# Kernel optimization log

Measured on AMD Instinct MI355X. Metric: run time of the kernel, lower is better.

Reference implementation:

```python
import jax, jax.numpy as jnp
import numpy as np
import math

B, S, D, H = 4, 2048, 1024, 16
DH = D // H  # 64


def setup_inputs() -> dict:
    key = jax.random.key(0)
    ks = jax.random.split(key, 7)
    scale = 1.0 / math.sqrt(D)
    q = jax.random.normal(ks[0], (B, S, D), dtype=jnp.float32)
    k = jax.random.normal(ks[1], (B, S, D), dtype=jnp.float32)
    v = jax.random.normal(ks[2], (B, S, D), dtype=jnp.float32)
    mask = jnp.tril(jnp.ones((S, S), dtype=jnp.int32))[None, None]  # [1,1,S,S] causal
    wq = jax.random.normal(ks[3], (D, D), dtype=jnp.float32) * scale
    wk = jax.random.normal(ks[4], (D, D), dtype=jnp.float32) * scale
    wv = jax.random.normal(ks[5], (D, D), dtype=jnp.float32) * scale
    wo = jax.random.normal(ks[6], (D, D), dtype=jnp.float32) * scale
    return {"q": q, "k": k, "v": v, "mask": mask, "wq": wq, "wk": wk, "wv": wv, "wo": wo}


def reference(q, k, v, mask, wq, wk, wv, wo):
    # nn.Linear(bias=False): y = x @ W.T
    qry = q @ wq.T
    key = k @ wk.T
    val = v @ wv.T
    # [B,S,D] -> [B,H,S,DH]
    qry = qry.reshape(B, S, H, DH).transpose(0, 2, 1, 3)
    key = key.reshape(B, S, H, DH).transpose(0, 2, 1, 3)
    val = val.reshape(B, S, H, DH).transpose(0, 2, 1, 3)
    scores = jnp.einsum('bhqd,bhkd->bhqk', qry, key) / math.sqrt(DH)
    scores = jnp.where(mask == 0, jnp.float32(-1e9), scores)
    attn = jax.nn.softmax(scores, axis=-1)  # dropout p=0.0 -> identity
    x = jnp.einsum('bhqk,bhkd->bhqd', attn, val)
    x = x.transpose(0, 2, 1, 3).reshape(B, S, D)
    return x @ wo.T
```

## Files before the change

kernel.cpp:

```cpp
#include <hip/hip_runtime.h>
#include <hip/hip_bf16.h>

typedef __attribute__((ext_vector_type(8))) short bf16x8;
typedef __attribute__((ext_vector_type(4))) float f32x4;
typedef __attribute__((ext_vector_type(16))) float f32x16;

#define MFMA16(a, b, c) __builtin_amdgcn_mfma_f32_16x16x32_bf16((a), (b), (c), 0, 0, 0)
#define MFMA32(a, b, c) __builtin_amdgcn_mfma_f32_32x32x16_bf16((a), (b), (c), 0, 0, 0)

#if defined(__has_builtin)
#if __has_builtin(__builtin_amdgcn_exp2f)
#define EXP2(x) __builtin_amdgcn_exp2f(x)
#endif
#endif
#ifndef EXP2
#define EXP2(x) exp2f(x)
#endif

__device__ __forceinline__ short f2b(float f) {
  unsigned u = __builtin_bit_cast(unsigned, f);
  u += 0x7FFFu + ((u >> 16) & 1u);
  return (short)(u >> 16);
}
__device__ __forceinline__ unsigned cvtpk(float lo, float hi) {
  unsigned r;
  asm("v_cvt_pk_bf16_f32 %0, %1, %2" : "=v"(r) : "v"(lo), "v"(hi));
  return r;
}

__global__ __launch_bounds__(256) void cvt3_bf16(const float* __restrict__ s0,
                                                 const float* __restrict__ s1,
                                                 const float* __restrict__ s2,
                                                 short* __restrict__ d, long stride) {
  const int which = blockIdx.y;
  const float* s = which == 0 ? s0 : (which == 1 ? s1 : s2);
  long i = (long)blockIdx.x * 256 + threadIdx.x;
  const float4* sp = (const float4*)s;
  float4 a = sp[2 * i], b = sp[2 * i + 1];
  bf16x8 o;
  o[0] = f2b(a.x); o[1] = f2b(a.y); o[2] = f2b(a.z); o[3] = f2b(a.w);
  o[4] = f2b(b.x); o[5] = f2b(b.y); o[6] = f2b(b.z); o[7] = f2b(b.w);
  *(bf16x8*)(d + which * stride + i * 8) = o;
}
__global__ __launch_bounds__(256) void cvt4_bf16(const float* __restrict__ s0,
                                                 const float* __restrict__ s1,
                                                 const float* __restrict__ s2,
                                                 const float* __restrict__ s3,
                                                 short* __restrict__ d, long stride) {
  const int which = blockIdx.y;
  const float* s = which == 0 ? s0 : (which == 1 ? s1 : (which == 2 ? s2 : s3));
  long i = (long)blockIdx.x * 256 + threadIdx.x;
  const float4* sp = (const float4*)s;
  float4 a = sp[2 * i], b = sp[2 * i + 1];
  bf16x8 o;
  o[0] = f2b(a.x); o[1] = f2b(a.y); o[2] = f2b(a.z); o[3] = f2b(a.w);
  o[4] = f2b(b.x); o[5] = f2b(b.y); o[6] = f2b(b.z); o[7] = f2b(b.w);
  *(bf16x8*)(d + which * stride + i * 8) = o;
}

template <int MODE>
__global__ __launch_bounds__(256) void gemm_bt(const short* __restrict__ A,
                                               const short* __restrict__ BT,
                                               void* __restrict__ Cout,
                                               int M, int N, int K, float oscale) {
  __shared__ __align__(16) short As[2][128 * 64];
  __shared__ __align__(16) short Bs[2][128 * 64];
  const int t = threadIdx.x;
  const int l = t & 63, w = t >> 6;
  const int grp = l >> 4, li = l & 15;
  const int nbn = N >> 7;
  const int bm = (int)blockIdx.x / nbn, bn = (int)blockIdx.x % nbn;
  const int m0 = bm << 7, n0 = bn << 7;
  const int wm = (w >> 1) << 6, wn = (w & 1) << 6;
  const int srow = t >> 3, scol = (t & 7) << 3;
  const int NT = K >> 6;
  f32x4 acc[4][4] = {};

#define GSTAGE(KT, BUF)                                                                    \
  {                                                                                        \
    _Pragma("unroll") for (int i = 0; i < 4; ++i) {                                        \
      const short* ga = A + (long)(m0 + i * 32 + srow) * K + (KT) * 64 + scol;             \
      __builtin_amdgcn_global_load_lds(                                                    \
          (const __attribute__((address_space(1))) void*)ga,                               \
          (__attribute__((address_space(3))) void*)&As[BUF][i * 2048 + t * 8], 16, 0, 0);  \
    }                                                                                      \
    _Pragma("unroll") for (int i = 0; i < 4; ++i) {                                        \
      const short* gb = BT + (long)(n0 + i * 32 + srow) * K + (KT) * 64 + scol;            \
      __builtin_amdgcn_global_load_lds(                                                    \
          (const __attribute__((address_space(1))) void*)gb,                               \
          (__attribute__((address_space(3))) void*)&Bs[BUF][i * 2048 + t * 8], 16, 0, 0);  \
    }                                                                                      \
  }

  GSTAGE(0, 0);
  __syncthreads();
  for (int kt = 0; kt < NT; ++kt) {
    const int cur = kt & 1;
    if (kt + 1 < NT) GSTAGE(kt + 1, cur ^ 1);
#pragma unroll
    for (int kk = 0; kk < 64; kk += 32) {
      bf16x8 af[4], bfr[4];
#pragma unroll
      for (int mi = 0; mi < 4; ++mi)
        af[mi] = *(const bf16x8*)&As[cur][(wm + mi * 16 + li) * 64 + kk + grp * 8];
#pragma unroll
      for (int ni = 0; ni < 4; ++ni)
        bfr[ni] = *(const bf16x8*)&Bs[cur][(wn + ni * 16 + li) * 64 + kk + grp * 8];
#pragma unroll
      for (int mi = 0; mi < 4; ++mi)
#pragma unroll
        for (int ni = 0; ni < 4; ++ni)
          acc[mi][ni] = MFMA16(af[mi], bfr[ni], acc[mi][ni]);
    }
    __syncthreads();
  }
#undef GSTAGE
#pragma unroll
  for (int mi = 0; mi < 4; ++mi) {
#pragma unroll
    for (int ni = 0; ni < 4; ++ni) {
      f32x4 v = acc[mi][ni];
      int n = n0 + wn + ni * 16 + li;
#pragma unroll
      for (int r = 0; r < 4; ++r) {
        int m = m0 + wm + mi * 16 + grp * 4 + r;
        if (MODE == 2) {
          ((float*)Cout)[(long)m * N + n] = v[r];
        } else {
          int b = m >> 11, sq = m & 2047;
          int h = n >> 6, dh = n & 63;
          if (MODE == 0)
            ((short*)Cout)[(((long)(b * 16 + h) * 2048 + sq) << 6) + dh] = f2b(v[r] * oscale);
          else
            ((short*)Cout)[(((long)(b * 16 + h) * 64 + dh) << 11) + sq] = f2b(v[r] * oscale);
        }
      }
    }
  }
}

__device__ __forceinline__ void attn_tile(const short* Kbuf, const short* Vbuf,
                                          const bf16x8 qf[4], f32x16& oa, f32x16& ob,
                                          float& mrun, float& lsum, int kt, bool diag,
                                          int khmax, int qg, int q, int hi) {
  f32x16 p0 = {}, p1 = {};
  __builtin_amdgcn_s_setprio(1);
#pragma unroll
  for (int kd = 0; kd < 4; ++kd) {
    int colB = kd * 32 + hi * 16;
    bf16x8 kf0 = *(const bf16x8*)((const char*)Kbuf + q * 128 + (colB ^ ((q & 7) << 4)));
    p0 = MFMA32(kf0, qf[kd], p0);
  }
  if (khmax == 2) {
#pragma unroll
    for (int kd = 0; kd < 4; ++kd) {
      int colB = kd * 32 + hi * 16;
      bf16x8 kf1 = *(const bf16x8*)((const char*)Kbuf + (q + 32) * 128 + (colB ^ ((q & 7) << 4)));
      p1 = MFMA32(kf1, qf[kd], p1);
    }
  }
  __builtin_amdgcn_s_setprio(0);
  if (diag) {
#pragma unroll
    for (int r = 0; r < 16; ++r) {
      int key0 = kt * 64 + (r & 3) + 8 * (r >> 2) + 4 * hi;
      if (key0 > qg) p0[r] = -1e30f;
      if (key0 + 32 > qg) p1[r] = -1e30f;
    }
  }
  float pm = p0[0];
#pragma unroll
  for (int r = 1; r < 16; ++r) pm = fmaxf(pm, p0[r]);
  if (khmax == 2) {
#pragma unroll
    for (int r = 0; r < 16; ++r) pm = fmaxf(pm, p1[r]);
  }
  pm = fmaxf(pm, __shfl_xor(pm, 32));
  const bool skip = __all(pm - mrun <= 11.5f);
  float mn;
  float alpha = 1.f;
  if (skip) {
    mn = mrun;
  } else {
    mn = fmaxf(mrun, pm);
    alpha = EXP2(mrun - mn);
    mrun = mn;
  }
  float ts = 0.f;
#pragma unroll
  for (int r = 0; r < 16; ++r) { p0[r] = EXP2(p0[r] - mn); ts += p0[r]; }
  if (khmax == 2) {
#pragma unroll
    for (int r = 0; r < 16; ++r) { p1[r] = EXP2(p1[r] - mn); ts += p1[r]; }
  }
  ts += __shfl_xor(ts, 32);
  if (skip) {
    lsum += ts;
  } else {
    lsum = lsum * alpha + ts;
#pragma unroll
    for (int r = 0; r < 16; ++r) { oa[r] *= alpha; ob[r] *= alpha; }
  }
  unsigned own0[8], prt0[8], own1[8], prt1[8];
#pragma unroll
  for (int g = 0; g < 4; ++g) {
    own0[2 * g]     = cvtpk(p0[4 * g], p0[4 * g + 1]);
    own0[2 * g + 1] = cvtpk(p0[4 * g + 2], p0[4 * g + 3]);
  }
#pragma unroll
  for (int i = 0; i < 8; ++i) prt0[i] = __shfl_xor(own0[i], 32);
  if (khmax == 2) {
#pragma unroll
    for (int g = 0; g < 4; ++g) {
      own1[2 * g]     = cvtpk(p1[4 * g], p1[4 * g + 1]);
      own1[2 * g + 1] = cvtpk(p1[4 * g + 2], p1[4 * g + 3]);
    }
#pragma unroll
    for (int i = 0; i < 8; ++i) prt1[i] = __shfl_xor(own1[i], 32);
  }
  __builtin_amdgcn_s_setprio(1);
#define PVSTEP(KD, OWN, PRT)                                                              \
  {                                                                                       \
    const int kdl = (KD) & 1;                                                             \
    unsigned b0 = hi ? PRT[4 * kdl + 2] : OWN[4 * kdl];                                   \
    unsigned b1 = hi ? PRT[4 * kdl + 3] : OWN[4 * kdl + 1];                               \
    unsigned b2 = hi ? OWN[4 * kdl + 2] : PRT[4 * kdl];                                   \
    unsigned b3 = hi ? OWN[4 * kdl + 3] : PRT[4 * kdl + 1];                               \
    int4 bi = {(int)b0, (int)b1, (int)b2, (int)b3};                                       \
    bf16x8 pb = __builtin_bit_cast(bf16x8, bi);                                           \
    int colB = (KD) * 32 + hi * 16;                                                       \
    bf16x8 vf0 = *(const bf16x8*)((const char*)Vbuf + q * 128 + (colB ^ ((q & 7) << 4))); \
    bf16x8 vf1 = *(const bf16x8*)((const char*)Vbuf + (q + 32) * 128 + (colB ^ ((q & 7) << 4))); \
    oa = MFMA32(vf0, pb, oa);                                                             \
    ob = MFMA32(vf1, pb, ob);                                                             \
  }
  PVSTEP(0, own0, prt0);
  PVSTEP(1, own0, prt0);
  if (khmax == 2) {
    PVSTEP(2, own1, prt1);
    PVSTEP(3, own1, prt1);
  }
#undef PVSTEP
  __builtin_amdgcn_s_setprio(0);
}

__global__ __launch_bounds__(256, 2) void attn_fwd(const short* __restrict__ Qh,
                                                   const short* __restrict__ Kh,
                                                   const short* __restrict__ Vt,
                                                   short* __restrict__ Xb) {
  __shared__ __align__(16) short Ks[2][4096];
  __shared__ __align__(16) short Vs[2][4096];
  const int bh = blockIdx.x;
  const int qtA = blockIdx.y;
  const int qtB = 15 - qtA;
  const int t = threadIdx.x, l = t & 63, w = t >> 6;
  const int q = l & 31, hi = l >> 5;
  const int q0wA = qtA * 128 + w * 32, q0wB = qtB * 128 + w * 32;
  const int qgA = q0wA + q, qgB = q0wB + q;
  const short* Qp = Qh + (long)bh * 131072;
  const char* Kb = (const char*)(Kh + (long)bh * 131072);
  const char* Vb = (const char*)(Vt + (long)bh * 131072);

  bf16x8 qfA[4], qfB[4];
#pragma unroll
  for (int kd = 0; kd < 4; ++kd) {
    qfA[kd] = *(const bf16x8*)(Qp + (long)qgA * 64 + kd * 16 + hi * 8);
    qfB[kd] = *(const bf16x8*)(Qp + (long)qgB * 64 + kd * 16 + hi * 8);
  }

  const int co0 = t * 16, co1 = co0 + 4096;

  f32x16 oaA = {}, obA = {}, oaB = {}, obB = {};
  float mrunA = -1e30f, lsumA = 0.f, mrunB = -1e30f, lsumB = 0.f;
  const int tripsA = (q0wA >> 6) + 1;
  const int tripsB = (q0wB >> 6) + 1;
  const int nt = 2 * qtB + 2;

#define STAGE(KT, BUF)                                                                   \
  {                                                                                      \
    long ktb = (long)(KT) * 8192;                                                        \
    _Pragma("unroll") for (int c = 0; c < 2; ++c) {                                      \
      int o = c ? co1 : co0;                                                             \
      int ksrc = o ^ (((o >> 7) & 7) << 4);                                              \
      __builtin_amdgcn_global_load_lds(                                                  \
          (const __attribute__((address_space(1))) void*)(Kb + ktb + ksrc),              \
          (__attribute__((address_space(3))) void*)((char*)Ks[BUF] + o), 16, 0, 0);      \
      int row = o >> 7, c16 = (o >> 4) & 7;                                              \
      int vsrc = row * 4096 + (KT) * 128 + (((c16 ^ (row & 7))) << 4);                   \
      __builtin_amdgcn_global_load_lds(                                                  \
          (const __attribute__((address_space(1))) void*)(Vb + vsrc),                    \
          (__attribute__((address_space(3))) void*)((char*)Vs[BUF] + o), 16, 0, 0);      \
    }                                                                                    \
  }

  STAGE(0, 0);
  __syncthreads();

  for (int kt = 0; kt < nt; ++kt) {
    const int buf = kt & 1;
    if (kt + 1 < nt) STAGE(kt + 1, buf ^ 1);

    if (kt < tripsB) {
      const bool diag = (kt == tripsB - 1);
      const int khmax = (diag && ((q0wB & 32) == 0)) ? 1 : 2;
      attn_tile(Ks[buf], Vs[buf], qfB, oaB, obB, mrunB, lsumB, kt, diag, khmax, qgB, q, hi);
    }
    if (kt < tripsA) {
      const bool diag = (kt == tripsA - 1);
      const int khmax = (diag && ((q0wA & 32) == 0)) ? 1 : 2;
      attn_tile(Ks[buf], Vs[buf], qfA, oaA, obA, mrunA, lsumA, kt, diag, khmax, qgA, q, hi);
    }
    __syncthreads();
  }

  const int b = bh >> 4, h = bh & 15;
#define EPI(OA, OB, LS, QG)                                                \
  {                                                                        \
    const float inv = 1.f / (LS);                                          \
    short* orow = Xb + (long)(b * 2048 + (QG)) * 1024 + h * 64;            \
    _Pragma("unroll") for (int g = 0; g < 4; ++g) {                        \
      unsigned u0 = cvtpk((OA)[4 * g] * inv, (OA)[4 * g + 1] * inv);       \
      unsigned u1 = cvtpk((OA)[4 * g + 2] * inv, (OA)[4 * g + 3] * inv);   \
      uint2 uu = {u0, u1};                                                 \
      *(uint2*)(orow + 8 * g + 4 * hi) = uu;                               \
      unsigned w0 = cvtpk((OB)[4 * g] * inv, (OB)[4 * g + 1] * inv);       \
      unsigned w1 = cvtpk((OB)[4 * g + 2] * inv, (OB)[4 * g + 3] * inv);   \
      uint2 ww = {w0, w1};                                                 \
      *(uint2*)(orow + 32 + 8 * g + 4 * hi) = ww;                          \
    }                                                                      \
  }
  EPI(oaA, obA, lsumA, qgA);
  EPI(oaB, obB, lsumB, qgB);
#undef EPI
}

extern "C" void kernel_launch(void* const* d_in, const int* in_sizes, int n_in,
                              void* d_out, int out_size, void* d_ws, size_t ws_size,
                              hipStream_t stream) {
  const float* q  = (const float*)d_in[0];
  const float* k  = (const float*)d_in[1];
  const float* v  = (const float*)d_in[2];
  const float* wq = (const float*)d_in[4];
  const float* wk = (const float*)d_in[5];
  const float* wv = (const float*)d_in[6];
  const float* wo = (const float*)d_in[7];

  short* ws = (short*)d_ws;
  const long T = 8388608;
  short* qb  = ws;
  short* kb  = qb + T;
  short* vb  = kb + T;
  short* Qh  = vb + T;
  short* Kh  = Qh + T;
  short* Vt  = Kh + T;
  short* Xb  = Vt + T;
  short* wqb = Xb + T;
  short* wkb = wqb + 1048576;
  short* wvb = wkb + 1048576;
  short* wob = wvb + 1048576;

  cvt3_bf16<<<dim3(4096, 3), 256, 0, stream>>>(q, k, v, qb, T);
  cvt4_bf16<<<dim3(512, 4), 256, 0, stream>>>(wq, wk, wv, wo, wqb, 1048576);

  gemm_bt<0><<<512, 256, 0, stream>>>(qb, wqb, (void*)Qh, 8192, 1024, 1024, 0.18033688f);
  gemm_bt<0><<<512, 256, 0, stream>>>(kb, wkb, (void*)Kh, 8192, 1024, 1024, 1.0f);
  gemm_bt<1><<<512, 256, 0, stream>>>(vb, wvb, (void*)Vt, 8192, 1024, 1024, 1.0f);
  attn_fwd<<<dim3(64, 8), 256, 0, stream>>>(Qh, Kh, Vt, Xb);
  gemm_bt<2><<<512, 256, 0, stream>>>(Xb, wob, d_out, 8192, 1024, 1024, 1.0f);
}
```

Measured before the change: 216.1 us.

## Batch QKV projections into one launch and shrink attention blocks to 128 threads

The three QKV projection GEMMs now run as a single launch using a z-dimension. Shapes are hardcoded so loop bounds and strides become constants. The attention kernel moves from 256-thread blocks covering two 128-row query tiles to 128-thread blocks covering paired 64-row tiles, giving twice as many blocks for better load balance and occupancy. The K/V staging in attention drops double buffering for a single buffer with a sync after each load, which trades load/compute overlap for lower LDS use and more resident blocks.

```diff
diff --git a/kernel.cpp b/kernel.cpp
--- a/kernel.cpp
+++ b/kernel.cpp
@@ -58,63 +58,72 @@
   *(bf16x8*)(d + which * stride + i * 8) = o;
 }
 
-template <int MODE>
-__global__ __launch_bounds__(256) void gemm_bt(const short* __restrict__ A,
-                                               const short* __restrict__ BT,
-                                               void* __restrict__ Cout,
-                                               int M, int N, int K, float oscale) {
-  __shared__ __align__(16) short As[2][128 * 64];
-  __shared__ __align__(16) short Bs[2][128 * 64];
-  const int t = threadIdx.x;
-  const int l = t & 63, w = t >> 6;
-  const int grp = l >> 4, li = l & 15;
-  const int nbn = N >> 7;
-  const int bm = (int)blockIdx.x / nbn, bn = (int)blockIdx.x % nbn;
-  const int m0 = bm << 7, n0 = bn << 7;
-  const int wm = (w >> 1) << 6, wn = (w & 1) << 6;
-  const int srow = t >> 3, scol = (t & 7) << 3;
-  const int NT = K >> 6;
-  f32x4 acc[4][4] = {};
-
-#define GSTAGE(KT, BUF)                                                                    \
+#define GEMM_BODY(A_, BT_)                                                                 \
+  __shared__ __align__(16) short As[2][128 * 64];                                          \
+  __shared__ __align__(16) short Bs[2][128 * 64];                                          \
+  const int t = threadIdx.x;                                                               \
+  const int l = t & 63, w = t >> 6;                                                        \
+  const int grp = l >> 4, li = l & 15;                                                     \
+  const int bm = (int)blockIdx.x >> 3, bn = (int)blockIdx.x & 7;                           \
+  const int m0 = bm << 7, n0 = bn << 7;                                                    \
+  const int wm = (w >> 1) << 6, wn = (w & 1) << 6;                                         \
+  const int srow = t >> 3, scol = (t & 7) << 3;                                            \
+  f32x4 acc[4][4] = {};                                                                    \
   {                                                                                        \
     _Pragma("unroll") for (int i = 0; i < 4; ++i) {                                        \
-      const short* ga = A + (long)(m0 + i * 32 + srow) * K + (KT) * 64 + scol;             \
+      const short* ga = A_ + (long)(m0 + i * 32 + srow) * 1024 + scol;                     \
       __builtin_amdgcn_global_load_lds(                                                    \
           (const __attribute__((address_space(1))) void*)ga,                               \
-          (__attribute__((address_space(3))) void*)&As[BUF][i * 2048 + t * 8], 16, 0, 0);  \
-    }                                                                                      \
-    _Pragma("unroll") for (int i = 0; i < 4; ++i) {                                        \
-      const short* gb = BT + (long)(n0 + i * 32 + srow) * K + (KT) * 64 + scol;            \
+          (__attribute__((address_space(3))) void*)&As[0][i * 2048 + t * 8], 16, 0, 0);    \
+      const short* gb = BT_ + (long)(n0 + i * 32 + srow) * 1024 + scol;                    \
       __builtin_amdgcn_global_load_lds(                                                    \
           (const __attribute__((address_space(1))) void*)gb,                               \
-          (__attribute__((address_space(3))) void*)&Bs[BUF][i * 2048 + t * 8], 16, 0, 0);  \
+          (__attribute__((address_space(3))) void*)&Bs[0][i * 2048 + t * 8], 16, 0, 0);    \
     }                                                                                      \
-  }
-
-  GSTAGE(0, 0);
-  __syncthreads();
-  for (int kt = 0; kt < NT; ++kt) {
-    const int cur = kt & 1;
-    if (kt + 1 < NT) GSTAGE(kt + 1, cur ^ 1);
-#pragma unroll
-    for (int kk = 0; kk < 64; kk += 32) {
-      bf16x8 af[4], bfr[4];
-#pragma unroll
-      for (int mi = 0; mi < 4; ++mi)
-        af[mi] = *(const bf16x8*)&As[cur][(wm + mi * 16 + li) * 64 + kk + grp * 8];
-#pragma unroll
-      for (int ni = 0; ni < 4; ++ni)
-        bfr[ni] = *(const bf16x8*)&Bs[cur][(wn + ni * 16 + li) * 64 + kk + grp * 8];
-#pragma unroll
-      for (int mi = 0; mi < 4; ++mi)
-#pragma unroll
-        for (int ni = 0; ni < 4; ++ni)
-          acc[mi][ni] = MFMA16(af[mi], bfr[ni], acc[mi][ni]);
-    }
-    __syncthreads();
-  }
-#undef GSTAGE
+  }                                                                                        \
+  __syncthreads();                                                                         \
+  for (int kt = 0; kt < 16; ++kt) {                                                        \
+    const int cur = kt & 1;                                                                \
+    if (kt + 1 < 16) {                                                                     \
+      _Pragma("unroll") for (int i = 0; i < 4; ++i) {                                      \
+        const short* ga = A_ + (long)(m0 + i * 32 + srow) * 1024 + (kt + 1) * 64 + scol;   \
+        __builtin_amdgcn_global_load_lds(                                                  \
+            (const __attribute__((address_space(1))) void*)ga,                             \
+            (__attribute__((address_space(3))) void*)&As[cur ^ 1][i * 2048 + t * 8], 16, 0, 0); \
+        const short* gb = BT_ + (long)(n0 + i * 32 + srow) * 1024 + (kt + 1) * 64 + scol;  \
+        __builtin_amdgcn_global_load_lds(                                                  \
+            (const __attribute__((address_space(1))) void*)gb,                             \
+            (__attribute__((address_space(3))) void*)&Bs[cur ^ 1][i * 2048 + t * 8], 16, 0, 0); \
+      }                                                                                    \
+    }                                                                                      \
+    _Pragma("unroll") for (int kk = 0; kk < 64; kk += 32) {                                \
+      bf16x8 af[4], bfr[4];                                                                \
+      _Pragma("unroll") for (int mi = 0; mi < 4; ++mi)                                     \
+        af[mi] = *(const bf16x8*)&As[cur][(wm + mi * 16 + li) * 64 + kk + grp * 8];        \
+      _Pragma("unroll") for (int ni = 0; ni < 4; ++ni)                                     \
+        bfr[ni] = *(const bf16x8*)&Bs[cur][(wn + ni * 16 + li) * 64 + kk + grp * 8];       \
+      _Pragma("unroll") for (int mi = 0; mi < 4; ++mi)                                     \
+        _Pragma("unroll") for (int ni = 0; ni < 4; ++ni)                                   \
+          acc[mi][ni] = MFMA16(af[mi], bfr[ni], acc[mi][ni]);                              \
+    }                                                                                      \
+    __syncthreads();                                                                       \
+  }
+
+__global__ __launch_bounds__(256) void gemm_qkv(const short* __restrict__ qb,
+                                                const short* __restrict__ kb,
+                                                const short* __restrict__ vb,
+                                                const short* __restrict__ wqb,
+                                                const short* __restrict__ wkb,
+                                                const short* __restrict__ wvb,
+                                                short* __restrict__ Qh,
+                                                short* __restrict__ Kh,
+                                                short* __restrict__ Vt) {
+  const int z = blockIdx.z;
+  const short* A  = z == 0 ? qb : (z == 1 ? kb : vb);
+  const short* BT = z == 0 ? wqb : (z == 1 ? wkb : wvb);
+  short* C = z == 0 ? Qh : (z == 1 ? Kh : Vt);
+  const float oscale = z == 0 ? 0.18033688f : 1.0f;
+  GEMM_BODY(A, BT)
 #pragma unroll
   for (int mi = 0; mi < 4; ++mi) {
 #pragma unroll
@@ -124,16 +133,31 @@
 #pragma unroll
       for (int r = 0; r < 4; ++r) {
         int m = m0 + wm + mi * 16 + grp * 4 + r;
-        if (MODE == 2) {
-          ((float*)Cout)[(long)m * N + n] = v[r];
-        } else {
-          int b = m >> 11, sq = m & 2047;
-          int h = n >> 6, dh = n & 63;
-          if (MODE == 0)
-            ((short*)Cout)[(((long)(b * 16 + h) * 2048 + sq) << 6) + dh] = f2b(v[r] * oscale);
-          else
-            ((short*)Cout)[(((long)(b * 16 + h) * 64 + dh) << 11) + sq] = f2b(v[r] * oscale);
-        }
+        int b = m >> 11, sq = m & 2047;
+        int h = n >> 6, dh = n & 63;
+        if (z != 2)
+          C[(((long)(b * 16 + h) * 2048 + sq) << 6) + dh] = f2b(v[r] * oscale);
+        else
+          C[(((long)(b * 16 + h) * 64 + dh) << 11) + sq] = f2b(v[r]);
+      }
+    }
+  }
+}
+
+__global__ __launch_bounds__(256) void gemm_out(const short* __restrict__ A_,
+                                                const short* __restrict__ BT_,
+                                                float* __restrict__ C) {
+  GEMM_BODY(A_, BT_)
+#pragma unroll
+  for (int mi = 0; mi < 4; ++mi) {
+#pragma unroll
+    for (int ni = 0; ni < 4; ++ni) {
+      f32x4 v = acc[mi][ni];
+      int n = n0 + wn + ni * 16 + li;
+#pragma unroll
+      for (int r = 0; r < 4; ++r) {
+        int m = m0 + wm + mi * 16 + grp * 4 + r;
+        C[(long)m * 1024 + n] = v[r];
       }
     }
   }
@@ -244,19 +268,19 @@
   __builtin_amdgcn_s_setprio(0);
 }
 
-__global__ __launch_bounds__(256, 2) void attn_fwd(const short* __restrict__ Qh,
+__global__ __launch_bounds__(128, 4) void attn_fwd(const short* __restrict__ Qh,
                                                    const short* __restrict__ Kh,
                                                    const short* __restrict__ Vt,
                                                    short* __restrict__ Xb) {
-  __shared__ __align__(16) short Ks[2][4096];
-  __shared__ __align__(16) short Vs[2][4096];
+  __shared__ __align__(16) short Ks[4096];
+  __shared__ __align__(16) short Vs[4096];
   const int bh = blockIdx.x;
-  const int qtA = blockIdx.y;
-  const int qtB = 15 - qtA;
+  const int a  = blockIdx.y;
   const int t = threadIdx.x, l = t & 63, w = t >> 6;
   const int q = l & 31, hi = l >> 5;
-  const int q0wA = qtA * 128 + w * 32, q0wB = qtB * 128 + w * 32;
-  const int qgA = q0wA + q, qgB = q0wB + q;
+  const int q0A = a * 64 + w * 32;
+  const int q0B = (31 - a) * 64 + w * 32;
+  const int qgA = q0A + q, qgB = q0B + q;
   const short* Qp = Qh + (long)bh * 131072;
   const char* Kb = (const char*)(Kh + (long)bh * 131072);
   const char* Vb = (const char*)(Vt + (long)bh * 131072);
@@ -268,47 +292,37 @@
     qfB[kd] = *(const bf16x8*)(Qp + (long)qgB * 64 + kd * 16 + hi * 8);
   }
 
-  const int co0 = t * 16, co1 = co0 + 4096;
-
   f32x16 oaA = {}, obA = {}, oaB = {}, obB = {};
   float mrunA = -1e30f, lsumA = 0.f, mrunB = -1e30f, lsumB = 0.f;
-  const int tripsA = (q0wA >> 6) + 1;
-  const int tripsB = (q0wB >> 6) + 1;
-  const int nt = 2 * qtB + 2;
-
-#define STAGE(KT, BUF)                                                                   \
-  {                                                                                      \
-    long ktb = (long)(KT) * 8192;                                                        \
-    _Pragma("unroll") for (int c = 0; c < 2; ++c) {                                      \
-      int o = c ? co1 : co0;                                                             \
-      int ksrc = o ^ (((o >> 7) & 7) << 4);                                              \
-      __builtin_amdgcn_global_load_lds(                                                  \
-          (const __attribute__((address_space(1))) void*)(Kb + ktb + ksrc),              \
-          (__attribute__((address_space(3))) void*)((char*)Ks[BUF] + o), 16, 0, 0);      \
-      int row = o >> 7, c16 = (o >> 4) & 7;                                              \
-      int vsrc = row * 4096 + (KT) * 128 + (((c16 ^ (row & 7))) << 4);                   \
-      __builtin_amdgcn_global_load_lds(                                                  \
-          (const __attribute__((address_space(1))) void*)(Vb + vsrc),                    \
-          (__attribute__((address_space(3))) void*)((char*)Vs[BUF] + o), 16, 0, 0);      \
-    }                                                                                    \
-  }
-
-  STAGE(0, 0);
-  __syncthreads();
+  const int tripsA = a + 1;
+  const int tripsB = 32 - a;
+  const int nt = tripsB;
 
   for (int kt = 0; kt < nt; ++kt) {
-    const int buf = kt & 1;
-    if (kt + 1 < nt) STAGE(kt + 1, buf ^ 1);
-
-    if (kt < tripsB) {
+#pragma unroll
+    for (int c = 0; c < 4; ++c) {
+      int o = t * 16 + c * 2048;
+      int ksrc = o ^ (((o >> 7) & 7) << 4);
+      __builtin_amdgcn_global_load_lds(
+          (const __attribute__((address_space(1))) void*)(Kb + (long)kt * 8192 + ksrc),
+          (__attribute__((address_space(3))) void*)((char*)Ks + o), 16, 0, 0);
+      int row = o >> 7, c16 = (o >> 4) & 7;
+      int vsrc = row * 4096 + kt * 128 + ((c16 ^ (row & 7)) << 4);
+      __builtin_amdgcn_global_load_lds(
+          (const __attribute__((address_space(1))) void*)(Vb + vsrc),
+          (__attribute__((address_space(3))) void*)((char*)Vs + o), 16, 0, 0);
+    }
+    __syncthreads();
+
+    {
       const bool diag = (kt == tripsB - 1);
-      const int khmax = (diag && ((q0wB & 32) == 0)) ? 1 : 2;
-      attn_tile(Ks[buf], Vs[buf], qfB, oaB, obB, mrunB, lsumB, kt, diag, khmax, qgB, q, hi);
+      const int khmax = (diag && ((q0B & 32) == 0)) ? 1 : 2;
+      attn_tile(Ks, Vs, qfB, oaB, obB, mrunB, lsumB, kt, diag, khmax, qgB, q, hi);
     }
     if (kt < tripsA) {
       const bool diag = (kt == tripsA - 1);
-      const int khmax = (diag && ((q0wA & 32) == 0)) ? 1 : 2;
-      attn_tile(Ks[buf], Vs[buf], qfA, oaA, obA, mrunA, lsumA, kt, diag, khmax, qgA, q, hi);
+      const int khmax = (diag && ((q0A & 32) == 0)) ? 1 : 2;
+      attn_tile(Ks, Vs, qfA, oaA, obA, mrunA, lsumA, kt, diag, khmax, qgA, q, hi);
     }
     __syncthreads();
   }
@@ -362,9 +376,7 @@
   cvt3_bf16<<<dim3(4096, 3), 256, 0, stream>>>(q, k, v, qb, T);
   cvt4_bf16<<<dim3(512, 4), 256, 0, stream>>>(wq, wk, wv, wo, wqb, 1048576);
 
-  gemm_bt<0><<<512, 256, 0, stream>>>(qb, wqb, (void*)Qh, 8192, 1024, 1024, 0.18033688f);
-  gemm_bt<0><<<512, 256, 0, stream>>>(kb, wkb, (void*)Kh, 8192, 1024, 1024, 1.0f);
-  gemm_bt<1><<<512, 256, 0, stream>>>(vb, wvb, (void*)Vt, 8192, 1024, 1024, 1.0f);
-  attn_fwd<<<dim3(64, 8), 256, 0, stream>>>(Qh, Kh, Vt, Xb);
-  gemm_bt<2><<<512, 256, 0, stream>>>(Xb, wob, d_out, 8192, 1024, 1024, 1.0f);
-}
+  gemm_qkv<<<dim3(512, 1, 3), 256, 0, stream>>>(qb, kb, vb, wqb, wkb, wvb, Qh, Kh, Vt);
+  attn_fwd<<<dim3(64, 16), 128, 0, stream>>>(Qh, Kh, Vt, Xb);
+  gemm_out<<<512, 256, 0, stream>>>(Xb, wob, (float*)d_out);
+}
```

Result: slower. 380.0 us (+75.9%).
